# Kernel tuning notes

Measured on AMD Instinct MI355X. Metric: run time of the kernel, lower is better.

## Reference

```python
import jax, jax.numpy as jnp
import numpy as np

K = 3      # deformable kernel size
PAD = 1    # padding for all 3x3 convs


def conv2d(x, w, b):
    y = jax.lax.conv_general_dilated(x, w, (1, 1), ((PAD, PAD), (PAD, PAD)),
                                     dimension_numbers=('NCHW', 'OIHW', 'NCHW'))
    return y + b[None, :, None, None]


def ln_channels(x, w, b, eps=1e-5):
    # Restormer 'WithBias' LayerNorm: normalize over channel dim of NCHW
    mu = jnp.mean(x, axis=1, keepdims=True)
    var = jnp.mean((x - mu) ** 2, axis=1, keepdims=True)
    return (x - mu) / jnp.sqrt(var + eps) * w[None, :, None, None] + b[None, :, None, None]


def deform_conv(x, offset, mask, weight, bias):
    # x: [B,Cin,H,W], offset: [B,2*K*K,H,W] (dy,dx interleaved), mask: [B,K*K,H,W]
    B, Cin, H, W = x.shape
    Kk = K * K
    off = offset.reshape(B, Kk, 2, H, W)
    dy, dx = off[:, :, 0], off[:, :, 1]                     # [B,Kk,H,W]
    ky, kx = jnp.meshgrid(jnp.arange(K), jnp.arange(K), indexing='ij')
    ky = (ky.reshape(-1) - PAD).astype(x.dtype)             # [Kk]
    kx = (kx.reshape(-1) - PAD).astype(x.dtype)
    py = jnp.arange(H, dtype=x.dtype)[None, None, :, None] + ky[None, :, None, None] + dy
    px = jnp.arange(W, dtype=x.dtype)[None, None, None, :] + kx[None, :, None, None] + dx
    y0 = jnp.floor(py); x0 = jnp.floor(px)
    wy1 = py - y0; wx1 = px - x0
    xf = x.reshape(B, Cin, H * W)

    def corner(yc, xc, wgt):
        valid = (yc >= 0) & (yc <= H - 1) & (xc >= 0) & (xc <= W - 1)
        yi = jnp.clip(yc, 0, H - 1).astype(jnp.int32)
        xi = jnp.clip(xc, 0, W - 1).astype(jnp.int32)
        idx = (yi * W + xi).reshape(B, -1)                  # [B, Kk*H*W]
        v = jax.vmap(lambda xb, ib: xb[:, ib])(xf, idx)     # [B, Cin, Kk*H*W]
        v = v.reshape(B, Cin, Kk, H, W)
        return v * (wgt * valid.astype(x.dtype))[:, None]

    sampled = (corner(y0, x0, (1 - wy1) * (1 - wx1))
               + corner(y0, x0 + 1, (1 - wy1) * wx1)
               + corner(y0 + 1, x0, wy1 * (1 - wx1))
               + corner(y0 + 1, x0 + 1, wy1 * wx1))         # [B,Cin,Kk,H,W]
    sampled = sampled * mask[:, None]                        # modulated (DCNv2)
    wk = weight.reshape(weight.shape[0], Cin, Kk)            # [Cout,Cin,Kk]
    out = jnp.einsum('bckhw,ock->bohw', sampled, wk)
    return out + bias[None, :, None, None]


def setup_inputs() -> dict:
    key = jax.random.key(0)
    ks = jax.random.split(key, 12)
    B, Ce, Cf, H, W = 4, 32, 64, 128, 128
    Cin, Kk = Ce + Cf, K * K
    d = {
        'f_evt_rec': jax.random.normal(ks[0], (B, Ce, H, W), jnp.float32),
        'f_efnet':   jax.random.normal(ks[1], (B, Cf, H, W), jnp.float32),
        'ln_evt_w': jnp.ones((Ce,), jnp.float32), 'ln_evt_b': jnp.zeros((Ce,), jnp.float32),
        'ln_ef_w':  jnp.ones((Cf,), jnp.float32), 'ln_ef_b':  jnp.zeros((Cf,), jnp.float32),
        'ln_al_w':  jnp.ones((Cf,), jnp.float32), 'ln_al_b':  jnp.zeros((Cf,), jnp.float32),
        'off_w': jax.random.normal(ks[2], (2 * Kk, Cin, K, K), jnp.float32) * 0.01,
        'off_b': jnp.zeros((2 * Kk,), jnp.float32),
        'mod_w': jax.random.normal(ks[3], (Kk, Cin, K, K), jnp.float32) * 0.01,
        'mod_b': jnp.zeros((Kk,), jnp.float32),
        'reg_w': jax.random.normal(ks[4], (Cf, Cin, K, K), jnp.float32) * 0.05,
        'reg_b': jnp.zeros((Cf,), jnp.float32),
        'stage_idx': 0,
    }
    return d


def reference(f_evt_rec, f_efnet, ln_evt_w, ln_evt_b, ln_ef_w, ln_ef_b,
              ln_al_w, ln_al_b, off_w, off_b, mod_w, mod_b, reg_w, reg_b, stage_idx):
    e = ln_channels(f_evt_rec, ln_evt_w, ln_evt_b)
    fe = ln_channels(f_efnet, ln_ef_w, ln_ef_b)
    ox = jnp.concatenate([e, fe], axis=1)                    # [B,96,H,W]
    offset = conv2d(ox, off_w, off_b)
    mask = 2.0 * jax.nn.sigmoid(conv2d(ox, mod_w, mod_b))
    al = deform_conv(ox, offset, mask, reg_w, reg_b)         # [B,64,H,W]
    al = jnp.where(al >= 0, al, 0.2 * al)                    # LeakyReLU(0.2)
    al = ln_channels(al, ln_al_w, ln_al_b)
    return al
```

## Files before the change

kernel.cpp:

```cpp
#include <hip/hip_runtime.h>
#include <hip/hip_bf16.h>

#define BATCH 4
#define HH 128
#define WW 128
#define CE 32
#define CF 64
#define CIN 96
#define COUT 64

typedef __bf16 bf16x8 __attribute__((ext_vector_type(8)));
typedef float f32x4 __attribute__((ext_vector_type(4)));
#define MFMA16(a, b, c) __builtin_amdgcn_mfma_f32_16x16x32_bf16(a, b, c, 0, 0, 0)
typedef union { uint4 u; bf16x8 v; } U8;

#define OX_BYTES   (BATCH * HH * WW * CIN * 2)
#define WCT_OFFB   OX_BYTES
#define WCT_BYTES  (27 * 32 * 32 * 2)
#define WKT_OFFB   (WCT_OFFB + WCT_BYTES)


__global__ __launch_bounds__(256) void ln_concat_prep(
    const float* __restrict__ evt, const float* __restrict__ efn,
    const float* __restrict__ w_e, const float* __restrict__ b_e,
    const float* __restrict__ w_f, const float* __restrict__ b_f,
    const float* __restrict__ off_w, const float* __restrict__ mod_w,
    const float* __restrict__ reg_w,
    __hip_bfloat16* __restrict__ ox,
    __hip_bfloat16* __restrict__ wcombT2,
    __hip_bfloat16* __restrict__ wkT2) {
  __shared__ float vals[64 * 97];
  __shared__ float part[4 * 64 * 4];
  __shared__ float stat[64 * 4];

  {
    int e = blockIdx.x * 256 + threadIdx.x;
    const int TOT1 = 27 * 32 * 32;
    const int TOT2 = 27 * 64 * 32;
    if (e < TOT1) {
      int r = e & 31, g = e >> 5;
      int oc = g & 31, tks = g >> 5;
      int tap = tks / 3, ks = tks % 3, c = ks * 32 + r;
      float v = 0.f;
      if (oc < 18)      v = off_w[(oc * CIN + c) * 9 + tap];
      else if (oc < 27) v = mod_w[((oc - 18) * CIN + c) * 9 + tap];
      wcombT2[e] = __float2bfloat16(v);
    } else if (e < TOT1 + TOT2) {
      int e2 = e - TOT1;
      int r = e2 & 31, g = e2 >> 5;
      int oc = g & 63, tks = g >> 6;
      int tap = tks / 3, ks = tks % 3, c = ks * 32 + r;
      wkT2[e2] = __float2bfloat16(reg_w[(oc * CIN + c) * 9 + tap]);
    }
  }

  int bid = blockIdx.x;
  int wg = (bid & 7) * 128 + (bid >> 3);
  int p0 = wg * 64;
  int b = p0 >> 14, y = (p0 >> 7) & 127, x0 = p0 & 127;
  int t = threadIdx.x, px = t & 63, g = t >> 6;

  float sE = 0.f, sE2 = 0.f, sF = 0.f, sF2 = 0.f;
  const float* pe = evt + (((size_t)b * CE) << 14) + (y << 7) + x0 + px;
#pragma unroll
  for (int j = 0; j < 8; ++j) {
    int c = g * 8 + j;
    float v = pe[(size_t)c << 14];
    vals[px * 97 + c] = v; sE += v; sE2 += v * v;
  }
  const float* pf = efn + (((size_t)b * CF) << 14) + (y << 7) + x0 + px;
#pragma unroll
  for (int j = 0; j < 16; ++j) {
    int c = g * 16 + j;
    float v = pf[(size_t)c << 14];
    vals[px * 97 + CE + c] = v; sF += v; sF2 += v * v;
  }
  {
    float4 p4 = {sE, sE2, sF, sF2};
    *(float4*)&part[(g * 64 + px) * 4] = p4;
  }
  __syncthreads();
  if (g == 0) {
    float aE = 0.f, aE2 = 0.f, aF = 0.f, aF2 = 0.f;
#pragma unroll
    for (int gg = 0; gg < 4; ++gg) {
      float4 p4 = *(const float4*)&part[(gg * 64 + px) * 4];
      aE += p4.x; aE2 += p4.y; aF += p4.z; aF2 += p4.w;
    }
    float muE = aE * (1.f / CE);
    float vE = aE2 * (1.f / CE) - muE * muE;
    float muF = aF * (1.f / CF);
    float vF = aF2 * (1.f / CF) - muF * muF;
    float4 s4 = {muE, rsqrtf(vE + 1e-5f), muF, rsqrtf(vF + 1e-5f)};
    *(float4*)&stat[px * 4] = s4;
  }
  __syncthreads();
  uint* orow = (uint*)(ox + (size_t)p0 * CIN);
#pragma unroll
  for (int i = 0; i < 12; ++i) {
    int e = i * 256 + t;
    int xx = e / 48, c = (e % 48) * 2;
    float v0 = vals[xx * 97 + c], v1 = vals[xx * 97 + c + 1];
    float mu, rs, lw0, lb0, lw1, lb1;
    if (c < CE) {
      mu = stat[xx * 4 + 0]; rs = stat[xx * 4 + 1];
      lw0 = w_e[c]; lb0 = b_e[c]; lw1 = w_e[c + 1]; lb1 = b_e[c + 1];
    } else {
      mu = stat[xx * 4 + 2]; rs = stat[xx * 4 + 3];
      lw0 = w_f[c - CE]; lb0 = b_f[c - CE]; lw1 = w_f[c + 1 - CE]; lb1 = b_f[c + 1 - CE];
    }
    float o0 = (v0 - mu) * rs * lw0 + lb0;
    float o1 = (v1 - mu) * rs * lw1 + lb1;
    __hip_bfloat16 h0 = __float2bfloat16(o0), h1 = __float2bfloat16(o1);
    orow[e] = ((uint)*(unsigned short*)&h1 << 16) | (uint)*(unsigned short*)&h0;
  }
}

__device__ __forceinline__ uint blend1(uint u0, uint u1, uint u2, uint u3,
                                       float w0, float w1, float w2, float w3) {
  float lo = w0 * __uint_as_float(u0 << 16) + w1 * __uint_as_float(u1 << 16)
           + w2 * __uint_as_float(u2 << 16) + w3 * __uint_as_float(u3 << 16);
  float hi = w0 * __uint_as_float(u0 & 0xffff0000u) + w1 * __uint_as_float(u1 & 0xffff0000u)
           + w2 * __uint_as_float(u2 & 0xffff0000u) + w3 * __uint_as_float(u3 & 0xffff0000u);
  __hip_bfloat16 bl = __float2bfloat16(lo), bh = __float2bfloat16(hi);
  return ((uint)*(unsigned short*)&bh << 16) | (uint)*(unsigned short*)&bl;
}

__global__ __launch_bounds__(64) void conv_deform_fused(
    const __hip_bfloat16* __restrict__ ox,
    const __hip_bfloat16* __restrict__ wct2,
    const __hip_bfloat16* __restrict__ wkt2,
    const float* __restrict__ off_b, const float* __restrict__ mod_b,
    const float* __restrict__ reg_b,
    const float* __restrict__ lnw, const float* __restrict__ lnb,
    float* __restrict__ out) {
  __shared__ float offm[16 * 28];
  __shared__ float outl[16 * 65];

  int bid = blockIdx.x;
  int wg = (bid & 7) * 512 + (bid >> 3);
  int p0 = wg * 16;
  int b = p0 >> 14, y = (p0 >> 7) & 127, x0 = p0 & 127;
  const __hip_bfloat16* oxb = ox + (((size_t)b) << 14) * CIN;

  int lane = threadIdx.x, lr = lane & 15, lg = lane >> 4;

  f32x4 cc0 = {0.f,0.f,0.f,0.f}, cc1 = {0.f,0.f,0.f,0.f};
#pragma unroll
  for (int tap = 0; tap < 9; ++tap) {
    int yy = y + tap / 3 - 1;
    int xx = x0 + lr + tap % 3 - 1;
    bool valid = ((unsigned)yy < 128u) && ((unsigned)xx < 128u);
    int cy = min(max(yy, 0), 127), cx = min(max(xx, 0), 127);
    const __hip_bfloat16* arow = oxb + (size_t)((cy << 7) + cx) * CIN + lg * 8;
#pragma unroll
    for (int ks = 0; ks < 3; ++ks) {
      U8 a, w0, w1;
      a.u = *(const uint4*)(arow + ks * 32);
      if (!valid) { a.u.x = 0; a.u.y = 0; a.u.z = 0; a.u.w = 0; }
      const __hip_bfloat16* wb = wct2 + (size_t)((tap * 3 + ks) * 32) * 32 + lg * 8;
      w0.u = *(const uint4*)(wb + lr * 32);
      w1.u = *(const uint4*)(wb + (16 + lr) * 32);
      cc0 = MFMA16(a.v, w0.v, cc0);
      cc1 = MFMA16(a.v, w1.v, cc1);
    }
  }
#pragma unroll
  for (int nt = 0; nt < 2; ++nt) {
    int oc = nt * 16 + lr;
    if (oc < 27) {
      float bia = (oc < 18) ? off_b[oc] : mod_b[oc - 18];
      f32x4 a = nt ? cc1 : cc0;
#pragma unroll
      for (int r = 0; r < 4; ++r) {
        float v = a[r] + bia;
        if (oc >= 18) v = 2.f / (1.f + __expf(-v));
        offm[(lg * 4 + r) * 28 + oc] = v;
      }
    }
  }
  __syncthreads();

  const float* om = offm + lr * 28;
  f32x4 ac0 = {0.f,0.f,0.f,0.f}, ac1 = {0.f,0.f,0.f,0.f};
  f32x4 ac2 = {0.f,0.f,0.f,0.f}, ac3 = {0.f,0.f,0.f,0.f};

  uint4 q[2][4];
  int   idx[2][4];
  float pwv[2][4];

#define PARAMS(T, S)                                                          \
  {                                                                           \
    float dyv = om[2 * (T)], dxv = om[2 * (T) + 1], mk = om[18 + (T)];        \
    float psy = (float)(y + (T) / 3 - 1) + dyv;                               \
    float psx = (float)(x0 + lr + (T) % 3 - 1) + dxv;                         \
    float fy = floorf(psy), fx = floorf(psx);                                 \
    float wy1 = psy - fy, wx1 = psx - fx;                                     \
    float wy0 = 1.f - wy1, wx0 = 1.f - wx1;                                   \
    int iy0 = (int)fy, ix0 = (int)fx, iy1 = iy0 + 1, ix1 = ix0 + 1;           \
    float vy0 = ((unsigned)iy0 < 128u) ? 1.f : 0.f;                           \
    float vy1 = ((unsigned)iy1 < 128u) ? 1.f : 0.f;                           \
    float vx0 = ((unsigned)ix0 < 128u) ? 1.f : 0.f;                           \
    float vx1 = ((unsigned)ix1 < 128u) ? 1.f : 0.f;                           \
    int cy0 = min(max(iy0, 0), 127), cy1 = min(max(iy1, 0), 127);             \
    int cx0 = min(max(ix0, 0), 127), cx1 = min(max(ix1, 0), 127);             \
    idx[S][0] = ((cy0 << 7) + cx0) * CIN;                                     \
    idx[S][1] = ((cy0 << 7) + cx1) * CIN;                                     \
    idx[S][2] = ((cy1 << 7) + cx0) * CIN;                                     \
    idx[S][3] = ((cy1 << 7) + cx1) * CIN;                                     \
    pwv[S][0] = wy0 * wx0 * vy0 * vx0 * mk;                                   \
    pwv[S][1] = wy0 * wx1 * vy0 * vx1 * mk;                                   \
    pwv[S][2] = wy1 * wx0 * vy1 * vx0 * mk;                                   \
    pwv[S][3] = wy1 * wx1 * vy1 * vx1 * mk;                                   \
  }

#define GATHER(QS, PS, KOFF)                                                  \
  {                                                                           \
    q[QS][0] = *(const uint4*)(oxb + idx[PS][0] + (KOFF));                    \
    q[QS][1] = *(const uint4*)(oxb + idx[PS][1] + (KOFF));                    \
    q[QS][2] = *(const uint4*)(oxb + idx[PS][2] + (KOFF));                    \
    q[QS][3] = *(const uint4*)(oxb + idx[PS][3] + (KOFF));                    \
  }

  PARAMS(0, 0);
  GATHER(0, 0, lg * 8);

#pragma unroll
  for (int cc = 0; cc < 27; ++cc) {
    const int tap = cc / 3, ks = cc % 3;
    const int cur = cc & 1, tp = tap & 1;
    const __hip_bfloat16* wb = wkt2 + (size_t)((tap * 3 + ks) * 64) * 32 + lg * 8;
    U8 b0, b1, b2, b3;
    b0.u = *(const uint4*)(wb + lr * 32);
    b1.u = *(const uint4*)(wb + (16 + lr) * 32);
    b2.u = *(const uint4*)(wb + (32 + lr) * 32);
    b3.u = *(const uint4*)(wb + (48 + lr) * 32);
    U8 fa;
    fa.u.x = blend1(q[cur][0].x, q[cur][1].x, q[cur][2].x, q[cur][3].x,
                    pwv[tp][0], pwv[tp][1], pwv[tp][2], pwv[tp][3]);
    fa.u.y = blend1(q[cur][0].y, q[cur][1].y, q[cur][2].y, q[cur][3].y,
                    pwv[tp][0], pwv[tp][1], pwv[tp][2], pwv[tp][3]);
    fa.u.z = blend1(q[cur][0].z, q[cur][1].z, q[cur][2].z, q[cur][3].z,
                    pwv[tp][0], pwv[tp][1], pwv[tp][2], pwv[tp][3]);
    fa.u.w = blend1(q[cur][0].w, q[cur][1].w, q[cur][2].w, q[cur][3].w,
                    pwv[tp][0], pwv[tp][1], pwv[tp][2], pwv[tp][3]);
    if (cc < 26) {
      const int nc = cc + 1, ntap = nc / 3, nks = nc % 3;
      const int nxt = nc & 1, ntp = ntap & 1;
      if (nks == 0) PARAMS(ntap, ntp);
      GATHER(nxt, ntp, nks * 32 + lg * 8);
    }
    ac0 = MFMA16(fa.v, b0.v, ac0);
    ac1 = MFMA16(fa.v, b1.v, ac1);
    ac2 = MFMA16(fa.v, b2.v, ac2);
    ac3 = MFMA16(fa.v, b3.v, ac3);
  }
#undef PARAMS
#undef GATHER

#pragma unroll
  for (int nt = 0; nt < 4; ++nt) {
    int oc = nt * 16 + lr;
    float bia = reg_b[oc];
    f32x4 a = (nt == 0) ? ac0 : (nt == 1) ? ac1 : (nt == 2) ? ac2 : ac3;
#pragma unroll
    for (int r = 0; r < 4; ++r) {
      float v = a[r] + bia;
      v = (v >= 0.f) ? v : 0.2f * v;
      outl[(lg * 4 + r) * 65 + oc] = v;
    }
  }
  __syncthreads();
  {
    int px2 = lane >> 2, part = lane & 3;
    float s = 0.f, s2 = 0.f;
#pragma unroll
    for (int j = 0; j < 16; ++j) {
      float v = outl[px2 * 65 + part * 16 + j];
      s += v; s2 += v * v;
    }
    s += __shfl_xor(s, 1); s2 += __shfl_xor(s2, 1);
    s += __shfl_xor(s, 2); s2 += __shfl_xor(s2, 2);
    float mu = s * (1.f / 64.f);
    float var = s2 * (1.f / 64.f) - mu * mu;
    float rs = rsqrtf(var + 1e-5f);
    size_t ob = (size_t)b * COUT * 16384 + (size_t)y * 128 + x0 + px2;
#pragma unroll
    for (int j = 0; j < 16; ++j) {
      int oc = part * 16 + j;
      float v = outl[px2 * 65 + oc];
      out[ob + (size_t)oc * 16384] = (v - mu) * rs * lnw[oc] + lnb[oc];
    }
  }
}

extern "C" void kernel_launch(void* const* d_in, const int* in_sizes, int n_in,
                              void* d_out, int out_size, void* d_ws, size_t ws_size,
                              hipStream_t stream) {
  const float* evt      = (const float*)d_in[0];
  const float* efn      = (const float*)d_in[1];
  const float* ln_evt_w = (const float*)d_in[2];
  const float* ln_evt_b = (const float*)d_in[3];
  const float* ln_ef_w  = (const float*)d_in[4];
  const float* ln_ef_b  = (const float*)d_in[5];
  const float* ln_al_w  = (const float*)d_in[6];
  const float* ln_al_b  = (const float*)d_in[7];
  const float* off_w    = (const float*)d_in[8];
  const float* off_b    = (const float*)d_in[9];
  const float* mod_w    = (const float*)d_in[10];
  const float* mod_b    = (const float*)d_in[11];
  const float* reg_w    = (const float*)d_in[12];
  const float* reg_b    = (const float*)d_in[13];
  float* out = (float*)d_out;

  char* wsb = (char*)d_ws;
  __hip_bfloat16* oxb    = (__hip_bfloat16*)wsb;
  __hip_bfloat16* wct2   = (__hip_bfloat16*)(wsb + WCT_OFFB);
  __hip_bfloat16* wkt2   = (__hip_bfloat16*)(wsb + WKT_OFFB);

  ln_concat_prep<<<BATCH * HH * WW / 64, 256, 0, stream>>>(
      evt, efn, ln_evt_w, ln_evt_b, ln_ef_w, ln_ef_b,
      off_w, mod_w, reg_w, oxb, wct2, wkt2);
  conv_deform_fused<<<BATCH * HH * WW / 16, 64, 0, stream>>>(
      oxb, wct2, wkt2, off_b, mod_b, reg_b, ln_al_w, ln_al_b, out);
}
```

Before: 186.3 us.

## Stage 5x69 input window in LDS for conv and deform gathers with 256-thread blocks

Blocks grow from 16 to 64 pixels (4 waves). Each block first loads a 5-row by 69-column by 96-channel window of the bf16 input into shared memory. The offset conv reads its taps from this window, and the bilinear gathers read from it when a corner falls inside, falling back to global memory otherwise. The goal is to replace scattered global gathers with LDS reads. The cost is about 66KB of LDS per block, which limits occupancy, plus an up-front window load and the loss of the software-pipelined gather prefetch.

```diff
diff --git a/kernel.cpp b/kernel.cpp
--- a/kernel.cpp
+++ b/kernel.cpp
@@ -126,7 +126,7 @@
   return ((uint)*(unsigned short*)&bh << 16) | (uint)*(unsigned short*)&bl;
 }
 
-__global__ __launch_bounds__(64) void conv_deform_fused(
+__global__ __launch_bounds__(256) void conv_deform_fused(
     const __hip_bfloat16* __restrict__ ox,
     const __hip_bfloat16* __restrict__ wct2,
     const __hip_bfloat16* __restrict__ wkt2,
@@ -134,35 +134,46 @@
     const float* __restrict__ reg_b,
     const float* __restrict__ lnw, const float* __restrict__ lnb,
     float* __restrict__ out) {
-  __shared__ float offm[16 * 28];
-  __shared__ float outl[16 * 65];
+  __shared__ short win[5 * 69 * CIN];
+  __shared__ float offm[64 * 28];
+  float* outl = (float*)win;
 
   int bid = blockIdx.x;
-  int wg = (bid & 7) * 512 + (bid >> 3);
-  int p0 = wg * 16;
+  int wg = (bid & 7) * 128 + (bid >> 3);
+  int p0 = wg * 64;
   int b = p0 >> 14, y = (p0 >> 7) & 127, x0 = p0 & 127;
   const __hip_bfloat16* oxb = ox + (((size_t)b) << 14) * CIN;
 
-  int lane = threadIdx.x, lr = lane & 15, lg = lane >> 4;
+  int t = threadIdx.x, lane = t & 63, wv = t >> 6;
+  int lr = lane & 15, lg = lane >> 4;
+  int pxw = (wv << 4) + lr;
+
+  for (int u = t; u < 5 * 69 * 12; u += 256) {
+    int c8 = u % 12, pos = u / 12;
+    int wr = pos / 69, wc = pos % 69;
+    int gy = y - 2 + wr, gx = x0 - 2 + wc;
+    uint4 v = {0u, 0u, 0u, 0u};
+    if ((unsigned)gy < 128u && (unsigned)gx < 128u)
+      v = *(const uint4*)(oxb + (size_t)((gy << 7) + gx) * CIN + c8 * 8);
+    *(uint4*)&win[pos * CIN + c8 * 8] = v;
+  }
+  __syncthreads();
 
   f32x4 cc0 = {0.f,0.f,0.f,0.f}, cc1 = {0.f,0.f,0.f,0.f};
 #pragma unroll
   for (int tap = 0; tap < 9; ++tap) {
-    int yy = y + tap / 3 - 1;
-    int xx = x0 + lr + tap % 3 - 1;
-    bool valid = ((unsigned)yy < 128u) && ((unsigned)xx < 128u);
-    int cy = min(max(yy, 0), 127), cx = min(max(xx, 0), 127);
-    const __hip_bfloat16* arow = oxb + (size_t)((cy << 7) + cx) * CIN + lg * 8;
+    int wr = tap / 3 + 1;
+    int wc = pxw + tap % 3 + 1;
+    const short* ar = &win[(wr * 69 + wc) * CIN + lg * 8];
 #pragma unroll
     for (int ks = 0; ks < 3; ++ks) {
-      U8 a, w0, w1;
-      a.u = *(const uint4*)(arow + ks * 32);
-      if (!valid) { a.u.x = 0; a.u.y = 0; a.u.z = 0; a.u.w = 0; }
+      bf16x8 a = *(const bf16x8*)(ar + ks * 32);
       const __hip_bfloat16* wb = wct2 + (size_t)((tap * 3 + ks) * 32) * 32 + lg * 8;
+      U8 w0, w1;
       w0.u = *(const uint4*)(wb + lr * 32);
       w1.u = *(const uint4*)(wb + (16 + lr) * 32);
-      cc0 = MFMA16(a.v, w0.v, cc0);
-      cc1 = MFMA16(a.v, w1.v, cc1);
+      cc0 = MFMA16(a, w0.v, cc0);
+      cc1 = MFMA16(a, w1.v, cc1);
     }
   }
 #pragma unroll
@@ -175,88 +186,75 @@
       for (int r = 0; r < 4; ++r) {
         float v = a[r] + bia;
         if (oc >= 18) v = 2.f / (1.f + __expf(-v));
-        offm[(lg * 4 + r) * 28 + oc] = v;
+        offm[((wv << 4) + (lg << 2) + r) * 28 + oc] = v;
       }
     }
   }
-  __syncthreads();
-
-  const float* om = offm + lr * 28;
+
+  const float* om = offm + pxw * 28;
   f32x4 ac0 = {0.f,0.f,0.f,0.f}, ac1 = {0.f,0.f,0.f,0.f};
   f32x4 ac2 = {0.f,0.f,0.f,0.f}, ac3 = {0.f,0.f,0.f,0.f};
 
-  uint4 q[2][4];
-  int   idx[2][4];
-  float pwv[2][4];
-
-#define PARAMS(T, S)                                                          \
-  {                                                                           \
-    float dyv = om[2 * (T)], dxv = om[2 * (T) + 1], mk = om[18 + (T)];        \
-    float psy = (float)(y + (T) / 3 - 1) + dyv;                               \
-    float psx = (float)(x0 + lr + (T) % 3 - 1) + dxv;                         \
-    float fy = floorf(psy), fx = floorf(psx);                                 \
-    float wy1 = psy - fy, wx1 = psx - fx;                                     \
-    float wy0 = 1.f - wy1, wx0 = 1.f - wx1;                                   \
-    int iy0 = (int)fy, ix0 = (int)fx, iy1 = iy0 + 1, ix1 = ix0 + 1;           \
-    float vy0 = ((unsigned)iy0 < 128u) ? 1.f : 0.f;                           \
-    float vy1 = ((unsigned)iy1 < 128u) ? 1.f : 0.f;                           \
-    float vx0 = ((unsigned)ix0 < 128u) ? 1.f : 0.f;                           \
-    float vx1 = ((unsigned)ix1 < 128u) ? 1.f : 0.f;                           \
-    int cy0 = min(max(iy0, 0), 127), cy1 = min(max(iy1, 0), 127);             \
-    int cx0 = min(max(ix0, 0), 127), cx1 = min(max(ix1, 0), 127);             \
-    idx[S][0] = ((cy0 << 7) + cx0) * CIN;                                     \
-    idx[S][1] = ((cy0 << 7) + cx1) * CIN;                                     \
-    idx[S][2] = ((cy1 << 7) + cx0) * CIN;                                     \
-    idx[S][3] = ((cy1 << 7) + cx1) * CIN;                                     \
-    pwv[S][0] = wy0 * wx0 * vy0 * vx0 * mk;                                   \
-    pwv[S][1] = wy0 * wx1 * vy0 * vx1 * mk;                                   \
-    pwv[S][2] = wy1 * wx0 * vy1 * vx0 * mk;                                   \
-    pwv[S][3] = wy1 * wx1 * vy1 * vx1 * mk;                                   \
-  }
-
-#define GATHER(QS, PS, KOFF)                                                  \
-  {                                                                           \
-    q[QS][0] = *(const uint4*)(oxb + idx[PS][0] + (KOFF));                    \
-    q[QS][1] = *(const uint4*)(oxb + idx[PS][1] + (KOFF));                    \
-    q[QS][2] = *(const uint4*)(oxb + idx[PS][2] + (KOFF));                    \
-    q[QS][3] = *(const uint4*)(oxb + idx[PS][3] + (KOFF));                    \
-  }
-
-  PARAMS(0, 0);
-  GATHER(0, 0, lg * 8);
-
-#pragma unroll
-  for (int cc = 0; cc < 27; ++cc) {
-    const int tap = cc / 3, ks = cc % 3;
-    const int cur = cc & 1, tp = tap & 1;
-    const __hip_bfloat16* wb = wkt2 + (size_t)((tap * 3 + ks) * 64) * 32 + lg * 8;
-    U8 b0, b1, b2, b3;
-    b0.u = *(const uint4*)(wb + lr * 32);
-    b1.u = *(const uint4*)(wb + (16 + lr) * 32);
-    b2.u = *(const uint4*)(wb + (32 + lr) * 32);
-    b3.u = *(const uint4*)(wb + (48 + lr) * 32);
-    U8 fa;
-    fa.u.x = blend1(q[cur][0].x, q[cur][1].x, q[cur][2].x, q[cur][3].x,
-                    pwv[tp][0], pwv[tp][1], pwv[tp][2], pwv[tp][3]);
-    fa.u.y = blend1(q[cur][0].y, q[cur][1].y, q[cur][2].y, q[cur][3].y,
-                    pwv[tp][0], pwv[tp][1], pwv[tp][2], pwv[tp][3]);
-    fa.u.z = blend1(q[cur][0].z, q[cur][1].z, q[cur][2].z, q[cur][3].z,
-                    pwv[tp][0], pwv[tp][1], pwv[tp][2], pwv[tp][3]);
-    fa.u.w = blend1(q[cur][0].w, q[cur][1].w, q[cur][2].w, q[cur][3].w,
-                    pwv[tp][0], pwv[tp][1], pwv[tp][2], pwv[tp][3]);
-    if (cc < 26) {
-      const int nc = cc + 1, ntap = nc / 3, nks = nc % 3;
-      const int nxt = nc & 1, ntp = ntap & 1;
-      if (nks == 0) PARAMS(ntap, ntp);
-      GATHER(nxt, ntp, nks * 32 + lg * 8);
-    }
-    ac0 = MFMA16(fa.v, b0.v, ac0);
-    ac1 = MFMA16(fa.v, b1.v, ac1);
-    ac2 = MFMA16(fa.v, b2.v, ac2);
-    ac3 = MFMA16(fa.v, b3.v, ac3);
-  }
-#undef PARAMS
-#undef GATHER
+#pragma unroll
+  for (int tap = 0; tap < 9; ++tap) {
+    float dyv = om[2 * tap], dxv = om[2 * tap + 1], mk = om[18 + tap];
+    float psy = (float)(y + tap / 3 - 1) + dyv;
+    float psx = (float)(x0 + pxw + tap % 3 - 1) + dxv;
+    float fy = floorf(psy), fx = floorf(psx);
+    float wy1 = psy - fy, wx1 = psx - fx;
+    float wy0 = 1.f - wy1, wx0 = 1.f - wx1;
+    int iy0 = (int)fy, ix0 = (int)fx, iy1 = iy0 + 1, ix1 = ix0 + 1;
+    float vy0 = ((unsigned)iy0 < 128u) ? 1.f : 0.f;
+    float vy1 = ((unsigned)iy1 < 128u) ? 1.f : 0.f;
+    float vx0 = ((unsigned)ix0 < 128u) ? 1.f : 0.f;
+    float vx1 = ((unsigned)ix1 < 128u) ? 1.f : 0.f;
+    int cy0 = min(max(iy0, 0), 127), cy1 = min(max(iy1, 0), 127);
+    int cx0 = min(max(ix0, 0), 127), cx1 = min(max(ix1, 0), 127);
+    float pw0 = wy0 * wx0 * vy0 * vx0 * mk;
+    float pw1 = wy0 * wx1 * vy0 * vx1 * mk;
+    float pw2 = wy1 * wx0 * vy1 * vx0 * mk;
+    float pw3 = wy1 * wx1 * vy1 * vx1 * mk;
+    int ra = cy0 - y + 2, rb = cy1 - y + 2;
+    int ca = cx0 - x0 + 2, cb = cx1 - x0 + 2;
+    bool ina = (unsigned)ra < 5u, inb = (unsigned)rb < 5u;
+    bool inca = (unsigned)ca < 69u, incb = (unsigned)cb < 69u;
+    int w0o = (ina && inca) ? (ra * 69 + ca) * CIN : -1;
+    int w1o = (ina && incb) ? (ra * 69 + cb) * CIN : -1;
+    int w2o = (inb && inca) ? (rb * 69 + ca) * CIN : -1;
+    int w3o = (inb && incb) ? (rb * 69 + cb) * CIN : -1;
+    int g0 = ((cy0 << 7) + cx0) * CIN, g1 = ((cy0 << 7) + cx1) * CIN;
+    int g2 = ((cy1 << 7) + cx0) * CIN, g3 = ((cy1 << 7) + cx1) * CIN;
+
+#pragma unroll
+    for (int ks = 0; ks < 3; ++ks) {
+      int koff = ks * 32 + lg * 8;
+      U8 q0, q1, q2, q3;
+      q0.v = *(const bf16x8*)&win[(w0o < 0 ? 0 : w0o) + koff];
+      q1.v = *(const bf16x8*)&win[(w1o < 0 ? 0 : w1o) + koff];
+      q2.v = *(const bf16x8*)&win[(w2o < 0 ? 0 : w2o) + koff];
+      q3.v = *(const bf16x8*)&win[(w3o < 0 ? 0 : w3o) + koff];
+      if (w0o < 0) q0.u = *(const uint4*)(oxb + g0 + koff);
+      if (w1o < 0) q1.u = *(const uint4*)(oxb + g1 + koff);
+      if (w2o < 0) q2.u = *(const uint4*)(oxb + g2 + koff);
+      if (w3o < 0) q3.u = *(const uint4*)(oxb + g3 + koff);
+      U8 fa;
+      fa.u.x = blend1(q0.u.x, q1.u.x, q2.u.x, q3.u.x, pw0, pw1, pw2, pw3);
+      fa.u.y = blend1(q0.u.y, q1.u.y, q2.u.y, q3.u.y, pw0, pw1, pw2, pw3);
+      fa.u.z = blend1(q0.u.z, q1.u.z, q2.u.z, q3.u.z, pw0, pw1, pw2, pw3);
+      fa.u.w = blend1(q0.u.w, q1.u.w, q2.u.w, q3.u.w, pw0, pw1, pw2, pw3);
+      const __hip_bfloat16* wb = wkt2 + (size_t)((tap * 3 + ks) * 64) * 32 + lg * 8;
+      U8 b0, b1, b2, b3;
+      b0.u = *(const uint4*)(wb + lr * 32);
+      b1.u = *(const uint4*)(wb + (16 + lr) * 32);
+      b2.u = *(const uint4*)(wb + (32 + lr) * 32);
+      b3.u = *(const uint4*)(wb + (48 + lr) * 32);
+      ac0 = MFMA16(fa.v, b0.v, ac0);
+      ac1 = MFMA16(fa.v, b1.v, ac1);
+      ac2 = MFMA16(fa.v, b2.v, ac2);
+      ac3 = MFMA16(fa.v, b3.v, ac3);
+    }
+  }
+  __syncthreads();
 
 #pragma unroll
   for (int nt = 0; nt < 4; ++nt) {
@@ -267,12 +265,11 @@
     for (int r = 0; r < 4; ++r) {
       float v = a[r] + bia;
       v = (v >= 0.f) ? v : 0.2f * v;
-      outl[(lg * 4 + r) * 65 + oc] = v;
-    }
-  }
-  __syncthreads();
+      outl[((wv << 4) + (lg << 2) + r) * 65 + oc] = v;
+    }
+  }
   {
-    int px2 = lane >> 2, part = lane & 3;
+    int px2 = (wv << 4) + (lane >> 2), part = lane & 3;
     float s = 0.f, s2 = 0.f;
 #pragma unroll
     for (int j = 0; j < 16; ++j) {
@@ -321,6 +318,6 @@
   ln_concat_prep<<<BATCH * HH * WW / 64, 256, 0, stream>>>(
       evt, efn, ln_evt_w, ln_evt_b, ln_ef_w, ln_ef_b,
       off_w, mod_w, reg_w, oxb, wct2, wkt2);
-  conv_deform_fused<<<BATCH * HH * WW / 16, 64, 0, stream>>>(
+  conv_deform_fused<<<BATCH * HH * WW / 64, 256, 0, stream>>>(
       oxb, wct2, wkt2, off_b, mod_b, reg_b, ln_al_w, ln_al_b, out);
 }
```

After: 167.4 us. 1.11x faster.

## Stage a 4x16 pixel halo window in LDS for conv and deformable gathers

Applied to the files above, without the earlier changes.

Each block now covers a 4-row by 16-column pixel tile with four waves instead of a single 16-pixel row with one wave. It first loads an 8x20 halo window of the bf16 activations into shared memory. The offset/mask convolution reads its A operands from that window with double-buffered weight loads. The bilinear gathers read from the window whenever the sample lands inside it and fall back to global memory otherwise. This is meant to cut redundant global gather traffic, at the cost of about 33 KB of LDS per block, which lowers occupancy, plus extra branching and per-sample index computation.

```diff
diff --git a/kernel.cpp b/kernel.cpp
--- a/kernel.cpp
+++ b/kernel.cpp
@@ -8,6 +8,11 @@
 #define CF 64
 #define CIN 96
 #define COUT 64
+
+#define WROWS 8
+#define WCOLS 20
+#define WSTR 104
+#define OFFSTR 27
 
 typedef __bf16 bf16x8 __attribute__((ext_vector_type(8)));
 typedef float f32x4 __attribute__((ext_vector_type(4)));
@@ -126,7 +131,7 @@
   return ((uint)*(unsigned short*)&bh << 16) | (uint)*(unsigned short*)&bl;
 }
 
-__global__ __launch_bounds__(64) void conv_deform_fused(
+__global__ __launch_bounds__(256) void conv_deform_fused(
     const __hip_bfloat16* __restrict__ ox,
     const __hip_bfloat16* __restrict__ wct2,
     const __hip_bfloat16* __restrict__ wkt2,
@@ -134,36 +139,62 @@
     const float* __restrict__ reg_b,
     const float* __restrict__ lnw, const float* __restrict__ lnb,
     float* __restrict__ out) {
-  __shared__ float offm[16 * 28];
-  __shared__ float outl[16 * 65];
+  __shared__ short win[WROWS * WCOLS * WSTR];
+  __shared__ float offm[64 * OFFSTR];
+  float* outl = (float*)win;
 
   int bid = blockIdx.x;
-  int wg = (bid & 7) * 512 + (bid >> 3);
-  int p0 = wg * 16;
-  int b = p0 >> 14, y = (p0 >> 7) & 127, x0 = p0 & 127;
+  int wg = (bid & 7) * 128 + (bid >> 3);
+  int b = wg >> 8;
+  int rem = wg & 255;
+  int y0 = (rem >> 3) << 2;
+  int x0 = (rem & 7) << 4;
   const __hip_bfloat16* oxb = ox + (((size_t)b) << 14) * CIN;
 
-  int lane = threadIdx.x, lr = lane & 15, lg = lane >> 4;
+  int t = threadIdx.x, lane = t & 63, wv = t >> 6;
+  int lr = lane & 15, lg = lane >> 4;
+  int pxrow = wv;
+  int pxcol = lr;
+
+  for (int u = t; u < WROWS * WCOLS * 12; u += 256) {
+    int c8 = u % 12, pos = u / 12;
+    int wr = pos / WCOLS, wc = pos % WCOLS;
+    int gy = y0 - 2 + wr, gx = x0 - 2 + wc;
+    uint4 v = {0u, 0u, 0u, 0u};
+    if ((unsigned)gy < 128u && (unsigned)gx < 128u)
+      v = *(const uint4*)(oxb + (size_t)((gy << 7) + gx) * CIN + c8 * 8);
+    *(uint4*)&win[pos * WSTR + c8 * 8] = v;
+  }
+  __syncthreads();
 
   f32x4 cc0 = {0.f,0.f,0.f,0.f}, cc1 = {0.f,0.f,0.f,0.f};
-#pragma unroll
-  for (int tap = 0; tap < 9; ++tap) {
-    int yy = y + tap / 3 - 1;
-    int xx = x0 + lr + tap % 3 - 1;
-    bool valid = ((unsigned)yy < 128u) && ((unsigned)xx < 128u);
-    int cy = min(max(yy, 0), 127), cx = min(max(xx, 0), 127);
-    const __hip_bfloat16* arow = oxb + (size_t)((cy << 7) + cx) * CIN + lg * 8;
-#pragma unroll
-    for (int ks = 0; ks < 3; ++ks) {
-      U8 a, w0, w1;
-      a.u = *(const uint4*)(arow + ks * 32);
-      if (!valid) { a.u.x = 0; a.u.y = 0; a.u.z = 0; a.u.w = 0; }
-      const __hip_bfloat16* wb = wct2 + (size_t)((tap * 3 + ks) * 32) * 32 + lg * 8;
-      w0.u = *(const uint4*)(wb + lr * 32);
-      w1.u = *(const uint4*)(wb + (16 + lr) * 32);
-      cc0 = MFMA16(a.v, w0.v, cc0);
-      cc1 = MFMA16(a.v, w1.v, cc1);
-    }
+  {
+    U8 cb0[2], cb1[2];
+    bf16x8 acur, anxt;
+#define CONV_ADDR(CC) ((pxrow + (CC)/3/1 + (CC)/3*0 + ((CC)/3) + 1) * 0)
+#define LDA_CONV(CC, DST)                                                   \
+    { int tp_ = (CC) / 3, ks_ = (CC) % 3;                                   \
+      int wr_ = pxrow + tp_ / 3 + 1, wc_ = pxcol + tp_ % 3 + 1;             \
+      (DST) = *(const bf16x8*)&win[(wr_ * WCOLS + wc_) * WSTR + ks_ * 32 + lg * 8]; }
+#define LDB_CONV(CC, Q)                                                     \
+    { const __hip_bfloat16* wb_ = wct2 + (size_t)(((CC)) * 32) * 32 + lg * 8; \
+      cb0[Q].u = *(const uint4*)(wb_ + lr * 32);                            \
+      cb1[Q].u = *(const uint4*)(wb_ + (16 + lr) * 32); }
+    LDA_CONV(0, acur);
+    LDB_CONV(0, 0);
+#pragma unroll
+    for (int cc = 0; cc < 27; ++cc) {
+      const int q = cc & 1;
+      if (cc < 26) {
+        LDB_CONV(cc + 1, q ^ 1);
+        LDA_CONV(cc + 1, anxt);
+      }
+      cc0 = MFMA16(acur, cb0[q].v, cc0);
+      cc1 = MFMA16(acur, cb1[q].v, cc1);
+      acur = anxt;
+    }
+#undef LDA_CONV
+#undef LDB_CONV
   }
 #pragma unroll
   for (int nt = 0; nt < 2; ++nt) {
@@ -175,25 +206,25 @@
       for (int r = 0; r < 4; ++r) {
         float v = a[r] + bia;
         if (oc >= 18) v = 2.f / (1.f + __expf(-v));
-        offm[(lg * 4 + r) * 28 + oc] = v;
+        offm[((wv << 4) + (lg << 2) + r) * OFFSTR + oc] = v;
       }
     }
   }
-  __syncthreads();
-
-  const float* om = offm + lr * 28;
+
+  const float* om = offm + ((wv << 4) + lr) * OFFSTR;
   f32x4 ac0 = {0.f,0.f,0.f,0.f}, ac1 = {0.f,0.f,0.f,0.f};
   f32x4 ac2 = {0.f,0.f,0.f,0.f}, ac3 = {0.f,0.f,0.f,0.f};
 
+  int widx[2][4], gidx[2][4];
+  float pw[2][4];
   uint4 q[2][4];
-  int   idx[2][4];
-  float pwv[2][4];
+  U8 bb0, bb1, bb2, bb3;
 
 #define PARAMS(T, S)                                                          \
   {                                                                           \
     float dyv = om[2 * (T)], dxv = om[2 * (T) + 1], mk = om[18 + (T)];        \
-    float psy = (float)(y + (T) / 3 - 1) + dyv;                               \
-    float psx = (float)(x0 + lr + (T) % 3 - 1) + dxv;                         \
+    float psy = (float)(y0 + pxrow + (T) / 3 - 1) + dyv;                      \
+    float psx = (float)(x0 + pxcol + (T) % 3 - 1) + dxv;                      \
     float fy = floorf(psy), fx = floorf(psx);                                 \
     float wy1 = psy - fy, wx1 = psx - fx;                                     \
     float wy0 = 1.f - wy1, wx0 = 1.f - wx1;                                   \
@@ -204,59 +235,74 @@
     float vx1 = ((unsigned)ix1 < 128u) ? 1.f : 0.f;                           \
     int cy0 = min(max(iy0, 0), 127), cy1 = min(max(iy1, 0), 127);             \
     int cx0 = min(max(ix0, 0), 127), cx1 = min(max(ix1, 0), 127);             \
-    idx[S][0] = ((cy0 << 7) + cx0) * CIN;                                     \
-    idx[S][1] = ((cy0 << 7) + cx1) * CIN;                                     \
-    idx[S][2] = ((cy1 << 7) + cx0) * CIN;                                     \
-    idx[S][3] = ((cy1 << 7) + cx1) * CIN;                                     \
-    pwv[S][0] = wy0 * wx0 * vy0 * vx0 * mk;                                   \
-    pwv[S][1] = wy0 * wx1 * vy0 * vx1 * mk;                                   \
-    pwv[S][2] = wy1 * wx0 * vy1 * vx0 * mk;                                   \
-    pwv[S][3] = wy1 * wx1 * vy1 * vx1 * mk;                                   \
-  }
-
-#define GATHER(QS, PS, KOFF)                                                  \
+    int ra = cy0 - y0 + 2, rb = cy1 - y0 + 2;                                 \
+    int ca = cx0 - x0 + 2, cb = cx1 - x0 + 2;                                 \
+    bool ina = (unsigned)ra < (unsigned)WROWS, inb = (unsigned)rb < (unsigned)WROWS; \
+    bool inca = (unsigned)ca < (unsigned)WCOLS, incb = (unsigned)cb < (unsigned)WCOLS; \
+    widx[S][0] = (ina && inca) ? (ra * WCOLS + ca) * WSTR : -1;               \
+    widx[S][1] = (ina && incb) ? (ra * WCOLS + cb) * WSTR : -1;               \
+    widx[S][2] = (inb && inca) ? (rb * WCOLS + ca) * WSTR : -1;               \
+    widx[S][3] = (inb && incb) ? (rb * WCOLS + cb) * WSTR : -1;               \
+    gidx[S][0] = ((cy0 << 7) + cx0) * CIN;                                    \
+    gidx[S][1] = ((cy0 << 7) + cx1) * CIN;                                    \
+    gidx[S][2] = ((cy1 << 7) + cx0) * CIN;                                    \
+    gidx[S][3] = ((cy1 << 7) + cx1) * CIN;                                    \
+    pw[S][0] = wy0 * wx0 * vy0 * vx0 * mk;                                    \
+    pw[S][1] = wy0 * wx1 * vy0 * vx1 * mk;                                    \
+    pw[S][2] = wy1 * wx0 * vy1 * vx0 * mk;                                    \
+    pw[S][3] = wy1 * wx1 * vy1 * vx1 * mk;                                    \
+  }
+
+#define LOADQ(KS, S, Q)                                                       \
   {                                                                           \
-    q[QS][0] = *(const uint4*)(oxb + idx[PS][0] + (KOFF));                    \
-    q[QS][1] = *(const uint4*)(oxb + idx[PS][1] + (KOFF));                    \
-    q[QS][2] = *(const uint4*)(oxb + idx[PS][2] + (KOFF));                    \
-    q[QS][3] = *(const uint4*)(oxb + idx[PS][3] + (KOFF));                    \
-  }
+    int koff_ = (KS) * 32 + lg * 8;                                           \
+    _Pragma("unroll")                                                         \
+    for (int j_ = 0; j_ < 4; ++j_) {                                          \
+      int w_ = widx[S][j_];                                                   \
+      U8 r_;                                                                  \
+      r_.v = *(const bf16x8*)&win[(w_ < 0 ? 0 : w_) + koff_];                 \
+      if (w_ < 0) r_.u = *(const uint4*)(oxb + gidx[S][j_] + koff_);          \
+      q[Q][j_] = r_.u;                                                        \
+    }                                                                         \
+  }
+
+#define LOADB(CC)                                                             \
+  { const __hip_bfloat16* wb_ = wkt2 + (size_t)((CC) * 64) * 32 + lg * 8;     \
+    bb0.u = *(const uint4*)(wb_ + lr * 32);                                   \
+    bb1.u = *(const uint4*)(wb_ + (16 + lr) * 32);                            \
+    bb2.u = *(const uint4*)(wb_ + (32 + lr) * 32);                            \
+    bb3.u = *(const uint4*)(wb_ + (48 + lr) * 32); }
 
   PARAMS(0, 0);
-  GATHER(0, 0, lg * 8);
-
+  LOADQ(0, 0, 0);
 #pragma unroll
   for (int cc = 0; cc < 27; ++cc) {
     const int tap = cc / 3, ks = cc % 3;
-    const int cur = cc & 1, tp = tap & 1;
-    const __hip_bfloat16* wb = wkt2 + (size_t)((tap * 3 + ks) * 64) * 32 + lg * 8;
-    U8 b0, b1, b2, b3;
-    b0.u = *(const uint4*)(wb + lr * 32);
-    b1.u = *(const uint4*)(wb + (16 + lr) * 32);
-    b2.u = *(const uint4*)(wb + (32 + lr) * 32);
-    b3.u = *(const uint4*)(wb + (48 + lr) * 32);
+    const int tp = tap & 1, qp = cc & 1;
+    LOADB(cc);
+    if (ks == 0 && tap < 8) PARAMS(tap + 1, tp ^ 1);
+    if (cc < 26) {
+      const int ntap = (cc + 1) / 3, nks = (cc + 1) % 3;
+      LOADQ(nks, ntap & 1, qp ^ 1);
+    }
     U8 fa;
-    fa.u.x = blend1(q[cur][0].x, q[cur][1].x, q[cur][2].x, q[cur][3].x,
-                    pwv[tp][0], pwv[tp][1], pwv[tp][2], pwv[tp][3]);
-    fa.u.y = blend1(q[cur][0].y, q[cur][1].y, q[cur][2].y, q[cur][3].y,
-                    pwv[tp][0], pwv[tp][1], pwv[tp][2], pwv[tp][3]);
-    fa.u.z = blend1(q[cur][0].z, q[cur][1].z, q[cur][2].z, q[cur][3].z,
-                    pwv[tp][0], pwv[tp][1], pwv[tp][2], pwv[tp][3]);
-    fa.u.w = blend1(q[cur][0].w, q[cur][1].w, q[cur][2].w, q[cur][3].w,
-                    pwv[tp][0], pwv[tp][1], pwv[tp][2], pwv[tp][3]);
-    if (cc < 26) {
-      const int nc = cc + 1, ntap = nc / 3, nks = nc % 3;
-      const int nxt = nc & 1, ntp = ntap & 1;
-      if (nks == 0) PARAMS(ntap, ntp);
-      GATHER(nxt, ntp, nks * 32 + lg * 8);
-    }
-    ac0 = MFMA16(fa.v, b0.v, ac0);
-    ac1 = MFMA16(fa.v, b1.v, ac1);
-    ac2 = MFMA16(fa.v, b2.v, ac2);
-    ac3 = MFMA16(fa.v, b3.v, ac3);
+    fa.u.x = blend1(q[qp][0].x, q[qp][1].x, q[qp][2].x, q[qp][3].x,
+                    pw[tp][0], pw[tp][1], pw[tp][2], pw[tp][3]);
+    fa.u.y = blend1(q[qp][0].y, q[qp][1].y, q[qp][2].y, q[qp][3].y,
+                    pw[tp][0], pw[tp][1], pw[tp][2], pw[tp][3]);
+    fa.u.z = blend1(q[qp][0].z, q[qp][1].z, q[qp][2].z, q[qp][3].z,
+                    pw[tp][0], pw[tp][1], pw[tp][2], pw[tp][3]);
+    fa.u.w = blend1(q[qp][0].w, q[qp][1].w, q[qp][2].w, q[qp][3].w,
+                    pw[tp][0], pw[tp][1], pw[tp][2], pw[tp][3]);
+    ac0 = MFMA16(fa.v, bb0.v, ac0);
+    ac1 = MFMA16(fa.v, bb1.v, ac1);
+    ac2 = MFMA16(fa.v, bb2.v, ac2);
+    ac3 = MFMA16(fa.v, bb3.v, ac3);
   }
 #undef PARAMS
-#undef GATHER
+#undef LOADQ
+#undef LOADB
+  __syncthreads();
 
 #pragma unroll
   for (int nt = 0; nt < 4; ++nt) {
@@ -267,12 +313,12 @@
     for (int r = 0; r < 4; ++r) {
       float v = a[r] + bia;
       v = (v >= 0.f) ? v : 0.2f * v;
-      outl[(lg * 4 + r) * 65 + oc] = v;
-    }
-  }
-  __syncthreads();
+      outl[((wv << 4) + (lg << 2) + r) * 65 + oc] = v;
+    }
+  }
   {
-    int px2 = lane >> 2, part = lane & 3;
+    int px2 = (wv << 4) + (lane >> 2), part = lane & 3;
+    int orow = (px2 >> 4), ocol = px2 & 15;
     float s = 0.f, s2 = 0.f;
 #pragma unroll
     for (int j = 0; j < 16; ++j) {
@@ -284,7 +330,7 @@
     float mu = s * (1.f / 64.f);
     float var = s2 * (1.f / 64.f) - mu * mu;
     float rs = rsqrtf(var + 1e-5f);
-    size_t ob = (size_t)b * COUT * 16384 + (size_t)y * 128 + x0 + px2;
+    size_t ob = (size_t)b * COUT * 16384 + (size_t)(y0 + orow) * 128 + x0 + ocol;
 #pragma unroll
     for (int j = 0; j < 16; ++j) {
       int oc = part * 16 + j;
@@ -321,6 +367,6 @@
   ln_concat_prep<<<BATCH * HH * WW / 64, 256, 0, stream>>>(
       evt, efn, ln_evt_w, ln_evt_b, ln_ef_w, ln_ef_b,
       off_w, mod_w, reg_w, oxb, wct2, wkt2);
-  conv_deform_fused<<<BATCH * HH * WW / 16, 64, 0, stream>>>(
+  conv_deform_fused<<<BATCH * HH * WW / 64, 256, 0, stream>>>(
       oxb, wct2, wkt2, off_b, mod_b, reg_b, ln_al_w, ln_al_b, out);
 }
```

After: 166.5 us. 1.12x faster.
